# Kernel optimization log

Hardware: AMD Instinct MI355X
Metric: run time of the kernel (lower is better)

The kernel has to match this reference:

```python
import jax, jax.numpy as jnp
import numpy as np

K = 3  # neighbor_k from init_kwargs
EPS = 0.0  # torch code does plain division by norm, no eps


def setup_inputs() -> dict:
    key = jax.random.key(0)
    k1, k2 = jax.random.split(key)
    q = jax.random.normal(k1, (128, 64, 21, 21), dtype=jnp.float32)   # [B, C, h, w]
    S = jax.random.normal(k2, (50, 64, 2205), dtype=jnp.float32)      # [n_way, C, M]
    return {"q": q, "S": S, "av_num": 1}


def reference(q, S, av_num):
    B, C, h, w = q.shape
    P = h * w
    # query descriptors: [B, P, C], L2-normalized per spatial descriptor (torch: norm over dim 1 of [P, C])
    qd = q.reshape(B, C, P).transpose(0, 2, 1)
    qn = qd / jnp.linalg.norm(qd, axis=-1, keepdims=True)

    def per_class(carry, Sj):
        # Sj: [C, M]; normalize each support descriptor (column) over C (torch: norm over dim 0)
        Sjn = Sj / jnp.linalg.norm(Sj, axis=0, keepdims=True)
        sim = jnp.einsum('bpc,cm->bpm', qn, Sjn)        # [B, P, M] cosine similarities
        topk = jax.lax.top_k(sim, K)[0]                  # top-k over support descriptors (last dim)
        return carry, topk.sum(axis=(1, 2))              # [B] image-to-class score

    _, sims = jax.lax.scan(per_class, None, S)           # [n_way, B]
    inner = sims.T                                       # [B, n_way]

    if av_num > 1:
        G = inner.shape[0] // av_num
        grp = inner.reshape(G, av_num, -1)
        return jnp.exp(jnp.mean(jnp.log(grp), axis=1))   # geometric mean over av group
    return inner
```

## Files before the change

### kernel.cpp

```cpp
#include <hip/hip_runtime.h>
#include <stdint.h>

typedef unsigned short u16;
typedef __attribute__((ext_vector_type(8))) short short8;
typedef __attribute__((ext_vector_type(4))) float f32x4;

#define MED3(a, b, c) __builtin_amdgcn_fmed3f((a), (b), (c))

static constexpr int Bn = 128, NWAY = 50, Cn = 64, Pn = 441, Mn = 2205;
static constexpr int PPAD = 448;
static constexpr int MPAD = 2240;
static constexpr int MT = 64;
static constexpr int NTILE = MPAD / MT;
static constexpr int NPF = 7;
static constexpr float NEG = -3.0e38f;

__device__ __forceinline__ u16 f2bf(float f) {
  union { float f; uint32_t u; } x; x.f = f;
  return (u16)((x.u + 0x7FFFu + ((x.u >> 16) & 1u)) >> 16);
}

__global__ void qnorm_kernel(const float* __restrict__ q, u16* __restrict__ qn) {
  int idx = blockIdx.x * 256 + threadIdx.x;
  if (idx >= Bn * PPAD) return;
  int b = idx / PPAD, p = idx - b * PPAD;
  u16* dst = qn + (size_t)idx * Cn;
  if (p >= Pn) {
    uint4 z = {0u, 0u, 0u, 0u};
#pragma unroll
    for (int c = 0; c < Cn; c += 8) *(uint4*)(dst + c) = z;
    return;
  }
  const float* src = q + (size_t)b * Cn * Pn + p;
  float v[Cn];
  float ss = 0.f;
#pragma unroll
  for (int c = 0; c < Cn; ++c) {
    float x = src[(size_t)c * Pn];
    v[c] = x;
    ss += x * x;
  }
  float inv = 1.0f / sqrtf(ss);
#pragma unroll
  for (int c = 0; c < Cn; c += 8) {
    uint4 w;
    w.x = (uint32_t)f2bf(v[c + 0] * inv) | ((uint32_t)f2bf(v[c + 1] * inv) << 16);
    w.y = (uint32_t)f2bf(v[c + 2] * inv) | ((uint32_t)f2bf(v[c + 3] * inv) << 16);
    w.z = (uint32_t)f2bf(v[c + 4] * inv) | ((uint32_t)f2bf(v[c + 5] * inv) << 16);
    w.w = (uint32_t)f2bf(v[c + 6] * inv) | ((uint32_t)f2bf(v[c + 7] * inv) << 16);
    *(uint4*)(dst + c) = w;
  }
}

__global__ void snorm_kernel(const float* __restrict__ S, u16* __restrict__ sn) {
  int idx = blockIdx.x * 256 + threadIdx.x;
  if (idx >= NWAY * MPAD) return;
  int j = idx / MPAD, m = idx - j * MPAD;
  u16* dst = sn + (size_t)idx * Cn;
  if (m >= Mn) {
    uint4 z = {0u, 0u, 0u, 0u};
#pragma unroll
    for (int c = 0; c < Cn; c += 8) *(uint4*)(dst + c) = z;
    return;
  }
  const float* src = S + (size_t)j * Cn * Mn + m;
  float v[Cn];
  float ss = 0.f;
#pragma unroll
  for (int c = 0; c < Cn; ++c) {
    float x = src[(size_t)c * Mn];
    v[c] = x;
    ss += x * x;
  }
  float inv = 1.0f / sqrtf(ss);
#pragma unroll
  for (int c = 0; c < Cn; c += 8) {
    uint4 w;
    w.x = (uint32_t)f2bf(v[c + 0] * inv) | ((uint32_t)f2bf(v[c + 1] * inv) << 16);
    w.y = (uint32_t)f2bf(v[c + 2] * inv) | ((uint32_t)f2bf(v[c + 3] * inv) << 16);
    w.z = (uint32_t)f2bf(v[c + 4] * inv) | ((uint32_t)f2bf(v[c + 5] * inv) << 16);
    w.w = (uint32_t)f2bf(v[c + 6] * inv) | ((uint32_t)f2bf(v[c + 7] * inv) << 16);
    *(uint4*)(dst + c) = w;
  }
}

#define STAGE(BUF, T)                                                          \
  do {                                                                         \
    const u16* _tile = Sj + (size_t)(T) * (MT * Cn);                           \
    __builtin_amdgcn_global_load_lds(                                          \
        (const __attribute__((address_space(1))) void*)(_tile + soff0),        \
        (__attribute__((address_space(3))) void*)(&sb[(BUF)][loff0]), 16, 0, 0);\
    __builtin_amdgcn_global_load_lds(                                          \
        (const __attribute__((address_space(1))) void*)(_tile + soff1),        \
        (__attribute__((address_space(3))) void*)(&sb[(BUF)][loff1]), 16, 0, 0);\
  } while (0)

#define COMPUTE_TILE(BASE0, BASE1, TAIL, TBASE)                                \
  do {                                                                         \
    _Pragma("unroll")                                                          \
    for (int mf = 0; mf < 4; ++mf) {                                           \
      short8 av0 = *(const short8*)((BASE0) + mf * 16 * Cn);                   \
      short8 av1 = *(const short8*)((BASE1) + mf * 16 * Cn);                   \
      _Pragma("unroll")                                                        \
      for (int pf = 0; pf < NPF; ++pf) {                                       \
        f32x4 acc =                                                            \
            __builtin_amdgcn_mfma_f32_16x16x32_bf16(av0, bq[pf][0], z4, 0, 0,  \
                                                    0);                        \
        acc = __builtin_amdgcn_mfma_f32_16x16x32_bf16(av1, bq[pf][1], acc, 0,  \
                                                      0, 0);                   \
        _Pragma("unroll")                                                      \
        for (int rr = 0; rr < 4; ++rr) {                                       \
          float v = acc[rr];                                                   \
          if (TAIL) {                                                          \
            if ((TBASE) + mf * 16 + lg4 + rr >= Mn) v = NEG;                   \
          }                                                                    \
          float o2 = MED3(t1[pf], t2[pf], v);                                  \
          float o1 = MED3(t0[pf], t1[pf], v);                                  \
          t0[pf] = fmaxf(t0[pf], v);                                           \
          t1[pf] = o1;                                                         \
          t2[pf] = o2;                                                         \
        }                                                                      \
      }                                                                        \
    }                                                                          \
  } while (0)

__global__ __launch_bounds__(256, 3) void knn_topk_kernel(
    const u16* __restrict__ qn, const u16* __restrict__ sn,
    float* __restrict__ out) {
  __shared__ __align__(16) u16 sb[2][MT * Cn];
  __shared__ float wsum[4];

  const int bid = blockIdx.x;
  const int b = bid / NWAY;
  const int j = bid - b * NWAY;
  const int tid = threadIdx.x;
  const int wave = tid >> 6;
  const int lane = tid & 63;
  const int lr = lane & 15;
  const int lg = lane >> 4;
  const int lg4 = lg * 4;

  const u16* Qb = qn + (size_t)b * PPAD * Cn;
  const u16* Sj = sn + (size_t)j * MPAD * Cn;

  const int q0 = tid, q1 = tid + 256;
  const int soff0 = ((q0 >> 3) * Cn) + ((((q0 & 7) ^ ((q0 >> 3) & 7))) * 8);
  const int soff1 = ((q1 >> 3) * Cn) + ((((q1 & 7) ^ ((q1 >> 3) & 7))) * 8);
  const int loff0 = q0 * 8, loff1 = q1 * 8;

  const int rs0 = ((0 + lg) ^ lr  ) * 8;
  const int rs1 = ((4 + lg) ^ (lr & 7)) * 8;
  const int rs0f = ((0 + lg) ^ (lr & 7)) * 8;
  const u16* rb0k0 = sb[0] + lr * Cn + rs0f;
  const u16* rb0k1 = sb[0] + lr * Cn + rs1;
  const u16* rb1k0 = sb[1] + lr * Cn + rs0f;
  const u16* rb1k1 = sb[1] + lr * Cn + rs1;
  (void)rs0;

  const f32x4 z4 = {0.f, 0.f, 0.f, 0.f};

  short8 bq[NPF][2];
  const int p_lane = wave * (NPF * 16) + lr;
#pragma unroll
  for (int pf = 0; pf < NPF; ++pf) {
    const u16* bp = Qb + (size_t)(p_lane + pf * 16) * Cn + lg * 8;
    bq[pf][0] = *(const short8*)(bp);
    bq[pf][1] = *(const short8*)(bp + 32);
  }

  float t0[NPF], t1[NPF], t2[NPF];
#pragma unroll
  for (int e = 0; e < NPF; ++e) { t0[e] = NEG; t1[e] = NEG; t2[e] = NEG; }

  STAGE(0, 0);
  __syncthreads();

  for (int t = 0; t < NTILE - 1; t += 2) {
    STAGE(1, t + 1);
    COMPUTE_TILE(rb0k0, rb0k1, 0, 0);
    __syncthreads();
    STAGE(0, t + 2);
    COMPUTE_TILE(rb1k0, rb1k1, 0, 0);
    __syncthreads();
  }
  COMPUTE_TILE(rb0k0, rb0k1, 1, (NTILE - 1) * MT);

  float total = 0.f;
#pragma unroll
  for (int pf = 0; pf < NPF; ++pf) {
    float a0 = t0[pf], a1 = t1[pf], a2 = t2[pf];
#pragma unroll
    for (int sh = 16; sh <= 32; sh <<= 1) {
      float b0 = __shfl_xor(a0, sh, 64);
      float b1 = __shfl_xor(a1, sh, 64);
      float b2 = __shfl_xor(a2, sh, 64);
      float n2 = MED3(a1, a2, b0);
      float n1 = MED3(a0, a1, b0);
      float n0 = fmaxf(a0, b0);
      n2 = MED3(n1, n2, b1);
      n1 = MED3(n0, n1, b1);
      n2 = MED3(n1, n2, b2);
      a0 = n0; a1 = n1; a2 = n2;
    }
    const int p = p_lane + pf * 16;
    if (lg == 0 && p < Pn) total += a0 + a1 + a2;
  }

#pragma unroll
  for (int sh = 1; sh <= 8; sh <<= 1) total += __shfl_xor(total, sh, 64);
  total += __shfl_xor(total, 16, 64);
  total += __shfl_xor(total, 32, 64);
  if (lane == 0) wsum[wave] = total;
  __syncthreads();
  if (tid == 0)
    out[(size_t)b * NWAY + j] = wsum[0] + wsum[1] + wsum[2] + wsum[3];
}

extern "C" void kernel_launch(void* const* d_in, const int* in_sizes, int n_in,
                              void* d_out, int out_size, void* d_ws,
                              size_t ws_size, hipStream_t stream) {
  (void)in_sizes; (void)n_in; (void)out_size; (void)ws_size;
  const float* q = (const float*)d_in[0];
  const float* S = (const float*)d_in[1];
  float* out = (float*)d_out;

  u16* qn = (u16*)d_ws;
  u16* sn = qn + (size_t)Bn * PPAD * Cn;

  qnorm_kernel<<<(Bn * PPAD) / 256, 256, 0, stream>>>(q, qn);
  snorm_kernel<<<(NWAY * MPAD + 255) / 256, 256, 0, stream>>>(S, sn);
  knn_topk_kernel<<<Bn * NWAY, 256, 0, stream>>>(qn, sn, out);
}
```

Baseline: 950.7 us.

## Share each support tile across two query images with 512-thread blocks

Each block now has 8 waves covering two batch images for one class. A staged support tile in LDS therefore feeds twice as many MFMAs, which halves global-to-LDS traffic and the number of blocks. The pipeline moves to 4 LDS buffers, staging two tiles ahead and computing two tiles between barriers. The cost is larger blocks that use more LDS and larger-scope barriers, with the occupancy target still set at 3 blocks per CU of 512 threads.

```diff
diff --git a/kernel.cpp b/kernel.cpp
--- a/kernel.cpp
+++ b/kernel.cpp
@@ -13,6 +13,7 @@
 static constexpr int MT = 64;
 static constexpr int NTILE = MPAD / MT;
 static constexpr int NPF = 7;
+static constexpr int TELEM = MT * Cn;
 static constexpr float NEG = -3.0e38f;
 
 __device__ __forceinline__ u16 f2bf(float f) {
@@ -86,21 +87,18 @@
 
 #define STAGE(BUF, T)                                                          \
   do {                                                                         \
-    const u16* _tile = Sj + (size_t)(T) * (MT * Cn);                           \
+    const u16* _tile = Sj + (size_t)(T) * TELEM;                               \
     __builtin_amdgcn_global_load_lds(                                          \
-        (const __attribute__((address_space(1))) void*)(_tile + soff0),        \
-        (__attribute__((address_space(3))) void*)(&sb[(BUF)][loff0]), 16, 0, 0);\
-    __builtin_amdgcn_global_load_lds(                                          \
-        (const __attribute__((address_space(1))) void*)(_tile + soff1),        \
-        (__attribute__((address_space(3))) void*)(&sb[(BUF)][loff1]), 16, 0, 0);\
+        (const __attribute__((address_space(1))) void*)(_tile + soff),         \
+        (__attribute__((address_space(3))) void*)(&sb[(BUF)][loff]), 16, 0, 0);\
   } while (0)
 
-#define COMPUTE_TILE(BASE0, BASE1, TAIL, TBASE)                                \
+#define COMPUTE_TILE(BO, TAIL, TBASE)                                          \
   do {                                                                         \
     _Pragma("unroll")                                                          \
     for (int mf = 0; mf < 4; ++mf) {                                           \
-      short8 av0 = *(const short8*)((BASE0) + mf * 16 * Cn);                   \
-      short8 av1 = *(const short8*)((BASE1) + mf * 16 * Cn);                   \
+      short8 av0 = *(const short8*)(rk0 + (BO) + mf * 16 * Cn);                \
+      short8 av1 = *(const short8*)(rk1 + (BO) + mf * 16 * Cn);                \
       _Pragma("unroll")                                                        \
       for (int pf = 0; pf < NPF; ++pf) {                                       \
         f32x4 acc =                                                            \
@@ -124,43 +122,41 @@
     }                                                                          \
   } while (0)
 
-__global__ __launch_bounds__(256, 3) void knn_topk_kernel(
+__global__ __launch_bounds__(512, 3) void knn_topk_kernel(
     const u16* __restrict__ qn, const u16* __restrict__ sn,
     float* __restrict__ out) {
-  __shared__ __align__(16) u16 sb[2][MT * Cn];
-  __shared__ float wsum[4];
+  __shared__ __align__(16) u16 sb[4][TELEM];
+  __shared__ float wsum[8];
 
   const int bid = blockIdx.x;
-  const int b = bid / NWAY;
-  const int j = bid - b * NWAY;
+  const int j = bid >> 6;
+  const int pair = bid & 63;
+  const int b0 = pair * 2;
+
   const int tid = threadIdx.x;
   const int wave = tid >> 6;
   const int lane = tid & 63;
   const int lr = lane & 15;
   const int lg = lane >> 4;
   const int lg4 = lg * 4;
-
-  const u16* Qb = qn + (size_t)b * PPAD * Cn;
+  const int bsel = wave >> 2;
+  const int wsub = wave & 3;
+
+  const u16* Qb = qn + (size_t)(b0 + bsel) * PPAD * Cn;
   const u16* Sj = sn + (size_t)j * MPAD * Cn;
 
-  const int q0 = tid, q1 = tid + 256;
-  const int soff0 = ((q0 >> 3) * Cn) + ((((q0 & 7) ^ ((q0 >> 3) & 7))) * 8);
-  const int soff1 = ((q1 >> 3) * Cn) + ((((q1 & 7) ^ ((q1 >> 3) & 7))) * 8);
-  const int loff0 = q0 * 8, loff1 = q1 * 8;
-
-  const int rs0 = ((0 + lg) ^ lr  ) * 8;
+  const int soff = ((tid >> 3) * Cn) + (((tid & 7) ^ ((tid >> 3) & 7)) * 8);
+  const int loff = tid * 8;
+
+  const int rs0 = ((0 + lg) ^ (lr & 7)) * 8;
   const int rs1 = ((4 + lg) ^ (lr & 7)) * 8;
-  const int rs0f = ((0 + lg) ^ (lr & 7)) * 8;
-  const u16* rb0k0 = sb[0] + lr * Cn + rs0f;
-  const u16* rb0k1 = sb[0] + lr * Cn + rs1;
-  const u16* rb1k0 = sb[1] + lr * Cn + rs0f;
-  const u16* rb1k1 = sb[1] + lr * Cn + rs1;
-  (void)rs0;
+  const u16* rk0 = sb[0] + lr * Cn + rs0;
+  const u16* rk1 = sb[0] + lr * Cn + rs1;
 
   const f32x4 z4 = {0.f, 0.f, 0.f, 0.f};
 
   short8 bq[NPF][2];
-  const int p_lane = wave * (NPF * 16) + lr;
+  const int p_lane = wsub * (NPF * 16) + lr;
 #pragma unroll
   for (int pf = 0; pf < NPF; ++pf) {
     const u16* bp = Qb + (size_t)(p_lane + pf * 16) * Cn + lg * 8;
@@ -173,17 +169,26 @@
   for (int e = 0; e < NPF; ++e) { t0[e] = NEG; t1[e] = NEG; t2[e] = NEG; }
 
   STAGE(0, 0);
+  STAGE(1, 1);
   __syncthreads();
 
-  for (int t = 0; t < NTILE - 1; t += 2) {
-    STAGE(1, t + 1);
-    COMPUTE_TILE(rb0k0, rb0k1, 0, 0);
+  for (int t = 0; t < 32; t += 4) {
+    STAGE(2, t + 2);
+    STAGE(3, t + 3);
+    COMPUTE_TILE(0, 0, 0);
+    COMPUTE_TILE(TELEM, 0, 0);
     __syncthreads();
-    STAGE(0, t + 2);
-    COMPUTE_TILE(rb1k0, rb1k1, 0, 0);
+    STAGE(0, t + 4);
+    STAGE(1, t + 5);
+    COMPUTE_TILE(2 * TELEM, 0, 0);
+    COMPUTE_TILE(3 * TELEM, 0, 0);
     __syncthreads();
   }
-  COMPUTE_TILE(rb0k0, rb0k1, 1, (NTILE - 1) * MT);
+  STAGE(2, 34);
+  COMPUTE_TILE(0, 0, 0);
+  COMPUTE_TILE(TELEM, 0, 0);
+  __syncthreads();
+  COMPUTE_TILE(2 * TELEM, 1, (NTILE - 1) * MT);
 
   float total = 0.f;
 #pragma unroll
@@ -191,15 +196,15 @@
     float a0 = t0[pf], a1 = t1[pf], a2 = t2[pf];
 #pragma unroll
     for (int sh = 16; sh <= 32; sh <<= 1) {
-      float b0 = __shfl_xor(a0, sh, 64);
-      float b1 = __shfl_xor(a1, sh, 64);
-      float b2 = __shfl_xor(a2, sh, 64);
-      float n2 = MED3(a1, a2, b0);
-      float n1 = MED3(a0, a1, b0);
-      float n0 = fmaxf(a0, b0);
-      n2 = MED3(n1, n2, b1);
-      n1 = MED3(n0, n1, b1);
-      n2 = MED3(n1, n2, b2);
+      float b0v = __shfl_xor(a0, sh, 64);
+      float b1v = __shfl_xor(a1, sh, 64);
+      float b2v = __shfl_xor(a2, sh, 64);
+      float n2 = MED3(a1, a2, b0v);
+      float n1 = MED3(a0, a1, b0v);
+      float n0 = fmaxf(a0, b0v);
+      n2 = MED3(n1, n2, b1v);
+      n1 = MED3(n0, n1, b1v);
+      n2 = MED3(n1, n2, b2v);
       a0 = n0; a1 = n1; a2 = n2;
     }
     const int p = p_lane + pf * 16;
@@ -212,8 +217,10 @@
   total += __shfl_xor(total, 32, 64);
   if (lane == 0) wsum[wave] = total;
   __syncthreads();
-  if (tid == 0)
-    out[(size_t)b * NWAY + j] = wsum[0] + wsum[1] + wsum[2] + wsum[3];
+  if (tid == 0) {
+    out[(size_t)b0 * NWAY + j] = wsum[0] + wsum[1] + wsum[2] + wsum[3];
+    out[(size_t)(b0 + 1) * NWAY + j] = wsum[4] + wsum[5] + wsum[6] + wsum[7];
+  }
 }
 
 extern "C" void kernel_launch(void* const* d_in, const int* in_sizes, int n_in,
@@ -229,5 +236,5 @@
 
   qnorm_kernel<<<(Bn * PPAD) / 256, 256, 0, stream>>>(q, qn);
   snorm_kernel<<<(NWAY * MPAD + 255) / 256, 256, 0, stream>>>(S, sn);
-  knn_topk_kernel<<<Bn * NWAY, 256, 0, stream>>>(qn, sn, out);
-}
+  knn_topk_kernel<<<NWAY * (Bn / 2), 512, 0, stream>>>(qn, sn, out);
+}
```

Result: no change. 965.0 us (+1.5%).
